# Optimization experiments

Measured on AMD Instinct MI355X. Metric: run time of the kernel, lower is better.

The kernel has to match this reference:

```python
import jax, jax.numpy as jnp
import numpy as np

B, S, E, H = 4, 512, 1024, 16
DH = E // H
SCALE = 1.0 / float(np.sqrt(DH))


def setup_inputs() -> dict:
    key = jax.random.key(0)
    ks = jax.random.split(key, 6)
    x_val = jax.random.normal(ks[0], (B, S, E), dtype=jnp.float32)
    eps = 0.1 * jax.random.uniform(ks[1], (B, S, E), dtype=jnp.float32)
    x_lb = x_val - eps
    x_ub = x_val + eps
    s = 1.0 / float(np.sqrt(E))
    in_proj_w = jax.random.uniform(ks[2], (E, 3 * E), jnp.float32, -s, s)
    in_proj_b = jax.random.uniform(ks[3], (3 * E,), jnp.float32, -s, s)
    out_proj_w = jax.random.uniform(ks[4], (E, E), jnp.float32, -s, s)
    out_proj_b = jax.random.uniform(ks[5], (E,), jnp.float32, -s, s)
    return dict(x_val=x_val, x_lb=x_lb, x_ub=x_ub,
                in_proj_w=in_proj_w, in_proj_b=in_proj_b,
                out_proj_w=out_proj_w, out_proj_b=out_proj_b)


def _pos(x):
    return jnp.maximum(x, 0.0)


def _neg(x):
    return jnp.minimum(x, 0.0)


def ibp_linear(v, l, u, W, b):
    # interval input x point weight: lb' = lb@W+ + ub@W-,  ub' = ub@W+ + lb@W-
    Wp, Wn = _pos(W), _neg(W)
    return v @ W + b, l @ Wp + u @ Wn + b, u @ Wp + l @ Wn + b


def ibp_matmul(av, al, au, bv, bl, bu):
    # interval x interval matmul with the 4-way clamp decomposition (as in ibp.matmul)
    val = av @ bv
    lb = (_pos(al) @ _pos(bl) + _pos(au) @ _neg(bl)
          + _neg(al) @ _pos(bu) + _neg(au) @ _neg(bu))
    ub = (_pos(au) @ _pos(bu) + _pos(al) @ _neg(bu)
          + _neg(au) @ _pos(bl) + _neg(al) @ _neg(bl))
    return val, lb, ub


def ibp_softmax(v, l, u):
    # p_i lower bound: exp(lb_i) / (exp(lb_i) + sum_{j!=i} exp(ub_j)); symmetric for upper
    pv = jax.nn.softmax(v, axis=-1)
    m = jnp.max(u, axis=-1, keepdims=True)
    e_l = jnp.exp(l - m)
    e_u = jnp.exp(u - m)
    S_l = jnp.sum(e_l, axis=-1, keepdims=True)
    S_u = jnp.sum(e_u, axis=-1, keepdims=True)
    pl = e_l / (S_u - e_u + e_l)
    pu = e_u / (S_l - e_l + e_u)
    return pv, jnp.clip(pl, 0.0, 1.0), jnp.clip(pu, 0.0, 1.0)


def _heads(x):  # [B,S,E] -> [B,H,S,DH]
    return x.reshape(B, S, H, DH).transpose(0, 2, 1, 3)


def _merge(x):  # [B,H,S,DH] -> [B,S,E]
    return x.transpose(0, 2, 1, 3).reshape(B, S, E)


def reference(x_val, x_lb, x_ub, in_proj_w, in_proj_b, out_proj_w, out_proj_b):
    qkv_v, qkv_l, qkv_u = ibp_linear(x_val, x_lb, x_ub, in_proj_w, in_proj_b)

    def split(t):
        q, k, v = jnp.split(t, 3, axis=-1)
        return _heads(q), _heads(k), _heads(v)

    (qv, kv, vv) = split(qkv_v)
    (ql, kl, vl) = split(qkv_l)
    (qu, ku, vu) = split(qkv_u)
    # positive scalar scale preserves bound ordering
    qv, ql, qu = qv * SCALE, ql * SCALE, qu * SCALE
    kT = lambda x: x.transpose(0, 1, 3, 2)
    sv, sl, su = ibp_matmul(qv, ql, qu, kT(kv), kT(kl), kT(ku))  # [B,H,S,S]
    pv, pl, pu = ibp_softmax(sv, sl, su)
    ov, ol, ou = ibp_matmul(pv, pl, pu, vv, vl, vu)  # [B,H,S,DH]
    ov, ol, ou = _merge(ov), _merge(ol), _merge(ou)
    yv, yl, yu = ibp_linear(ov, ol, ou, out_proj_w, out_proj_b)
    return jnp.stack([yv, yl, yu])  # [3,B,S,E]
```

## Files before the change

### kernel.cpp

```cpp
#include <hip/hip_runtime.h>
#include <math.h>

#define SEQ    512
#define EMB    1024
#define NHEAD  16
#define DHEAD  64
#define NBAT   4
#define QSCALE 0.125f
#define KS     72
#define VS     40

typedef __attribute__((ext_vector_type(8))) short bf16x8;
typedef __attribute__((ext_vector_type(4))) float f32x4;

#define MFMA16(a, b, c) __builtin_amdgcn_mfma_f32_16x16x32_bf16(a, b, c, 0, 0, 0)

__device__ __forceinline__ unsigned short f2b(float x) {
  union { float f; unsigned int u; } a; a.f = x;
  unsigned int u = a.u;
  unsigned int r = (u + 0x7fffu + ((u >> 16) & 1u)) >> 16;
  return (unsigned short)r;
}
__device__ __forceinline__ unsigned short f2b_fast(float x) {
  union { float f; unsigned int u; } a; a.f = x;
  return (unsigned short)((a.u + 0x8000u) >> 16);
}
__device__ __forceinline__ float b2f(unsigned short x) {
  union { unsigned int u; float f; } a; a.u = ((unsigned int)x) << 16; return a.f;
}

__device__ __forceinline__ void async16(const unsigned short* g, unsigned short* lds) {
  __builtin_amdgcn_global_load_lds(
      (const __attribute__((address_space(1))) unsigned int*)g,
      (__attribute__((address_space(3))) unsigned int*)lds, 16, 0, 0);
}

__device__ __forceinline__ void clamp_pn8(bf16x8 x, bf16x8* p, bf16x8* n) {
  const unsigned int* xu = (const unsigned int*)&x;
  unsigned int* pp = (unsigned int*)p;
  unsigned int* nn = (unsigned int*)n;
#pragma unroll
  for (int e = 0; e < 4; e++) {
    const unsigned int s = xu[e] & 0x80008000u;
    const unsigned int mask = s | (s - (s >> 15));
    nn[e] = xu[e] & mask;
    pp[e] = xu[e] & ~mask;
  }
}

__device__ __forceinline__ float wave16_sum(float x) {
#pragma unroll
  for (int m = 1; m <= 8; m <<= 1) x += __shfl_xor(x, m);
  return x;
}

__global__ __launch_bounds__(256)
void convert_stack(const float* __restrict__ v, const float* __restrict__ l,
                   const float* __restrict__ u,
                   unsigned short* __restrict__ outV,
                   unsigned short* __restrict__ outC,
                   unsigned short* __restrict__ outR, int total4)
{
  int i = blockIdx.x * 256 + threadIdx.x;
  if (i >= total4) return;
  float4 v4 = ((const float4*)v)[i];
  float4 l4 = ((const float4*)l)[i];
  float4 u4 = ((const float4*)u)[i];
  float lv[4] = {l4.x, l4.y, l4.z, l4.w};
  float uv[4] = {u4.x, u4.y, u4.z, u4.w};
  float vv[4] = {v4.x, v4.y, v4.z, v4.w};
  ushort4 ov, oc, orr;
  unsigned short* pv = (unsigned short*)&ov;
  unsigned short* pc = (unsigned short*)&oc;
  unsigned short* pr = (unsigned short*)&orr;
#pragma unroll
  for (int e = 0; e < 4; e++) {
    pv[e] = f2b(vv[e]);
    pc[e] = f2b(0.5f * (lv[e] + uv[e]));
    pr[e] = f2b(0.5f * (uv[e] - lv[e]));
  }
  ((ushort4*)outV)[i] = ov;
  ((ushort4*)outC)[i] = oc;
  ((ushort4*)outR)[i] = orr;
}

__global__ __launch_bounds__(256)
void wt_convert(const float* __restrict__ W,
                unsigned short* __restrict__ Wt,
                unsigned short* __restrict__ Wa, int K, int N)
{
  __shared__ float tile[32][33];
  const int n0 = blockIdx.x * 32, k0 = blockIdx.y * 32;
  const int tx = threadIdx.x, ty = threadIdx.y;
#pragma unroll
  for (int r = 0; r < 32; r += 8)
    tile[ty + r][tx] = W[(size_t)(k0 + ty + r) * N + n0 + tx];
  __syncthreads();
#pragma unroll
  for (int r = 0; r < 32; r += 8) {
    const float w = tile[tx][ty + r];
    const size_t o = (size_t)(n0 + ty + r) * K + k0 + tx;
    Wt[o] = f2b(w);
    Wa[o] = f2b(fabsf(w));
  }
}

template<int BN>
__global__ __launch_bounds__(256, 2)
void gemm_ibp3(const unsigned short* __restrict__ Av,
               const unsigned short* __restrict__ Ac,
               const unsigned short* __restrict__ Ar,
               const unsigned short* __restrict__ Bt,
               const unsigned short* __restrict__ Ba,
               int K, const float* __restrict__ bias,
               float* __restrict__ oV, float* __restrict__ oL, float* __restrict__ oU,
               unsigned short* __restrict__ hV, unsigned short* __restrict__ hL,
               unsigned short* __restrict__ hU,
               unsigned short* __restrict__ vtV, unsigned short* __restrict__ vtL,
               unsigned short* __restrict__ vtU, int N)
{
  constexpr int NF = BN / 32;
  __shared__ __attribute__((aligned(16))) unsigned short Avs[2][64 * 32];
  __shared__ __attribute__((aligned(16))) unsigned short Acs[2][64 * 32];
  __shared__ __attribute__((aligned(16))) unsigned short Ars[2][64 * 32];
  __shared__ __attribute__((aligned(16))) unsigned short Bts[2][BN * 32];
  __shared__ __attribute__((aligned(16))) unsigned short Bas[2][BN * 32];

  const int t = threadIdx.x, lane = t & 63, w = t >> 6;
  const int m0 = blockIdx.y * 64, n0 = blockIdx.x * BN;
  const int wm = w & 1, wn = w >> 1;
  const int quad = lane >> 4, r16 = lane & 15;
  const int srow = lane >> 2, sseg = lane & 3;

  f32x4 av[2][NF], ac[2][NF], ar[2][NF];
#pragma unroll
  for (int i = 0; i < 2; i++)
#pragma unroll
    for (int j = 0; j < NF; j++) {
      av[i][j] = (f32x4){0.f, 0.f, 0.f, 0.f};
      ac[i][j] = (f32x4){0.f, 0.f, 0.f, 0.f};
      ar[i][j] = (f32x4){0.f, 0.f, 0.f, 0.f};
    }

  const int iters = K >> 5;
  auto stage = [&](int it, int buf) {
    const int k0 = it * 32;
    const size_t ga = (size_t)(m0 + 16 * w + srow) * K + k0 + sseg * 8;
    async16(Av + ga, &Avs[buf][16 * w * 32]);
    async16(Ac + ga, &Acs[buf][16 * w * 32]);
    async16(Ar + ga, &Ars[buf][16 * w * 32]);
#pragma unroll
    for (int r = 0; r < BN / 64; r++) {
      const int brow = (BN / 4) * w + 16 * r;
      const size_t gb = (size_t)(n0 + brow + srow) * K + k0 + sseg * 8;
      async16(Bt + gb, &Bts[buf][brow * 32]);
      async16(Ba + gb, &Bas[buf][brow * 32]);
    }
  };

  stage(0, 0);
  for (int it = 0; it < iters; ++it) {
    const int cur = it & 1;
    __syncthreads();
    if (it + 1 < iters) stage(it + 1, cur ^ 1);
    bf16x8 fv[2], fc[2], fr[2], gt[NF], gb[NF];
#pragma unroll
    for (int i = 0; i < 2; i++) {
      const int off = (wm * 32 + i * 16 + r16) * 32 + quad * 8;
      fv[i] = *(const bf16x8*)(&Avs[cur][off]);
      fc[i] = *(const bf16x8*)(&Acs[cur][off]);
      fr[i] = *(const bf16x8*)(&Ars[cur][off]);
    }
#pragma unroll
    for (int j = 0; j < NF; j++) {
      const int off = (wn * (BN / 2) + j * 16 + r16) * 32 + quad * 8;
      gt[j] = *(const bf16x8*)(&Bts[cur][off]);
      gb[j] = *(const bf16x8*)(&Bas[cur][off]);
    }
#pragma unroll
    for (int i = 0; i < 2; i++)
#pragma unroll
      for (int j = 0; j < NF; j++) {
        av[i][j] = MFMA16(fv[i], gt[j], av[i][j]);
        ac[i][j] = MFMA16(fc[i], gt[j], ac[i][j]);
        ar[i][j] = MFMA16(fr[i], gb[j], ar[i][j]);
      }
  }

#pragma unroll
  for (int i = 0; i < 2; i++) {
    const int mbase = m0 + wm * 32 + i * 16 + quad * 4;
#pragma unroll
    for (int j = 0; j < NF; j++) {
      const int n = n0 + wn * (BN / 2) + j * 16 + r16;
      const float bv = bias[n];
      float vv[4], lv[4], uv[4];
#pragma unroll
      for (int rI = 0; rI < 4; rI++) {
        const float c = ac[i][j][rI], r = ar[i][j][rI];
        vv[rI] = av[i][j][rI] + bv;
        lv[rI] = c - r + bv;
        uv[rI] = c + r + bv;
      }
      if (hV) {
#pragma unroll
        for (int rI = 0; rI < 4; rI++) {
          hV[(size_t)(mbase + rI) * N + n] = f2b(vv[rI]);
          hL[(size_t)(mbase + rI) * N + n] = f2b(lv[rI]);
          hU[(size_t)(mbase + rI) * N + n] = f2b(uv[rI]);
        }
      } else {
#pragma unroll
        for (int rI = 0; rI < 4; rI++) {
          oV[(size_t)(mbase + rI) * N + n] = vv[rI];
          oL[(size_t)(mbase + rI) * N + n] = lv[rI];
          oU[(size_t)(mbase + rI) * N + n] = uv[rI];
        }
      }
      if (vtV && n >= 2048) {
        const int hh = (n - 2048) >> 6, dd = (n - 2048) & 63;
        const int bb = mbase >> 9, ss = mbase & 511;
        ushort4 v4, l4, u4;
        unsigned short* vp = (unsigned short*)&v4;
        unsigned short* lp = (unsigned short*)&l4;
        unsigned short* up = (unsigned short*)&u4;
#pragma unroll
        for (int rI = 0; rI < 4; rI++) {
          vp[rI] = f2b(vv[rI]); lp[rI] = f2b(lv[rI]); up[rI] = f2b(uv[rI]);
        }
        const size_t vo = (size_t)((bb * 16 + hh) * 64 + dd) * 512 + ss;
        *(ushort4*)(vtV + vo) = v4;
        *(ushort4*)(vtL + vo) = l4;
        *(ushort4*)(vtU + vo) = u4;
      }
    }
  }
}

__device__ __forceinline__ void qk_tile(const unsigned short* K0,
                                        const unsigned short* K1,
                                        const unsigned short* K2,
                                        int cl, int quad,
                                        const bf16x8 qvf[2], const bf16x8 qlpf[2],
                                        const bf16x8 qlnf[2], const bf16x8 qupf[2],
                                        const bf16x8 qunf[2],
                                        f32x4* avp, f32x4* alp, f32x4* aup)
{
  f32x4 v = {0.f, 0.f, 0.f, 0.f}, l = v, u = v;
#pragma unroll
  for (int kh = 0; kh < 2; kh++) {
    const int off = cl * KS + kh * 32 + quad * 8;
    bf16x8 kv = *(const bf16x8*)(K0 + off);
    bf16x8 kl = *(const bf16x8*)(K1 + off);
    bf16x8 ku = *(const bf16x8*)(K2 + off);
    bf16x8 klp, kln, kup, kun;
    clamp_pn8(kl, &klp, &kln);
    clamp_pn8(ku, &kup, &kun);
    v = MFMA16(qvf[kh], kv, v);
    l = MFMA16(qlpf[kh], klp, l);
    l = MFMA16(qupf[kh], kln, l);
    l = MFMA16(qlnf[kh], kup, l);
    l = MFMA16(qunf[kh], kun, l);
    u = MFMA16(qupf[kh], kup, u);
    u = MFMA16(qlpf[kh], kun, u);
    u = MFMA16(qunf[kh], klp, u);
    u = MFMA16(qlnf[kh], kln, u);
  }
  *avp = v; *alp = l; *aup = u;
}

__global__ __launch_bounds__(256, 4)
void ibp_attn_mfma(const unsigned short* __restrict__ qkv_v,
                   const unsigned short* __restrict__ qkv_l,
                   const unsigned short* __restrict__ qkv_u,
                   const unsigned short* __restrict__ vt_v,
                   const unsigned short* __restrict__ vt_l,
                   const unsigned short* __restrict__ vt_u,
                   unsigned short* __restrict__ Ov,
                   unsigned short* __restrict__ Oc,
                   unsigned short* __restrict__ Or)
{
  __shared__ __attribute__((aligned(16))) unsigned short pool[6912 + 7680 + 3840];
  __shared__ float st[2][32][3];
  unsigned short* Ks = pool;
  unsigned short* Vs = pool + 6912;
  unsigned short* Ps = pool + 6912 + 7680;

  const int qblk = blockIdx.x, h = blockIdx.y, b = blockIdx.z;
  const int t = threadIdx.x, lane = t & 63, w = t >> 6;
  const int wm = w >> 1, wc = w & 1;
  const int quad = lane >> 4, r16 = lane & 15;
  const int mq = b * SEQ + qblk * 32;
  const int bh = b * NHEAD + h;

  bf16x8 qvf[2], qlpf[2], qlnf[2], qupf[2], qunf[2];
  {
    const size_t qrow = (size_t)(mq + wm * 16 + r16) * 3072 + h * 64;
#pragma unroll
    for (int kh = 0; kh < 2; kh++) {
      bf16x8 v8 = *(const bf16x8*)(qkv_v + qrow + kh * 32 + quad * 8);
      bf16x8 l8 = *(const bf16x8*)(qkv_l + qrow + kh * 32 + quad * 8);
      bf16x8 u8 = *(const bf16x8*)(qkv_u + qrow + kh * 32 + quad * 8);
      const unsigned short* vs = (const unsigned short*)&v8;
      const unsigned short* ls = (const unsigned short*)&l8;
      const unsigned short* us = (const unsigned short*)&u8;
      unsigned short* ov = (unsigned short*)&qvf[kh];
      unsigned short* lp = (unsigned short*)&qlpf[kh];
      unsigned short* ln = (unsigned short*)&qlnf[kh];
      unsigned short* up = (unsigned short*)&qupf[kh];
      unsigned short* un = (unsigned short*)&qunf[kh];
#pragma unroll
      for (int e = 0; e < 8; e++) {
        ov[e] = f2b(b2f(vs[e]) * QSCALE);
        const float lf = b2f(ls[e]) * QSCALE;
        const float uf = b2f(us[e]) * QSCALE;
        lp[e] = f2b(fmaxf(lf, 0.f)); ln[e] = f2b(fminf(lf, 0.f));
        up[e] = f2b(fmaxf(uf, 0.f)); un[e] = f2b(fminf(uf, 0.f));
      }
    }
  }

  const int cl = wc * 16 + r16;
  const int krow = t >> 3, kseg = t & 7;
  const int vrow = t >> 2, vseg = t & 3;
  const unsigned short* kplane[3] = {qkv_v, qkv_l, qkv_u};
  const unsigned short* vplane[3] = {vt_v, vt_l, vt_u};

  float Svp[4] = {0.f, 0.f, 0.f, 0.f};
  float Slp[4] = {0.f, 0.f, 0.f, 0.f};
  float Sup[4] = {0.f, 0.f, 0.f, 0.f};

#pragma unroll
  for (int pI = 0; pI < 3; pI++)
    *(uint4*)(Ks + pI * 2304 + krow * KS + kseg * 8) =
        *(const uint4*)(kplane[pI] + (size_t)(b * SEQ + krow) * 3072 + 1024 + h * 64 + kseg * 8);
  __syncthreads();

  for (int ct = 0; ct < 16; ct++) {
    const unsigned short* cur = (ct & 1) ? Vs : Ks;
    if (ct < 15) {
      unsigned short* nxt = (ct & 1) ? Ks : Vs;
      const int c0n = (ct + 1) * 32;
#pragma unroll
      for (int pI = 0; pI < 3; pI++)
        *(uint4*)(nxt + pI * 2304 + krow * KS + kseg * 8) =
            *(const uint4*)(kplane[pI] + (size_t)(b * SEQ + c0n + krow) * 3072 + 1024 + h * 64 + kseg * 8);
    }
    f32x4 av, al, au;
    qk_tile(cur, cur + 2304, cur + 4608, cl, quad,
            qvf, qlpf, qlnf, qupf, qunf, &av, &al, &au);
#pragma unroll
    for (int r = 0; r < 4; r++) {
      Svp[r] += __expf(av[r]);
      Slp[r] += __expf(al[r]);
      Sup[r] += __expf(au[r]);
    }
    __syncthreads();
  }

#pragma unroll
  for (int r = 0; r < 4; r++) {
    Svp[r] = wave16_sum(Svp[r]);
    Slp[r] = wave16_sum(Slp[r]);
    Sup[r] = wave16_sum(Sup[r]);
  }
  if (r16 == 0) {
#pragma unroll
    for (int r = 0; r < 4; r++) {
      st[wc][wm * 16 + quad * 4 + r][0] = Svp[r];
      st[wc][wm * 16 + quad * 4 + r][1] = Slp[r];
      st[wc][wm * 16 + quad * 4 + r][2] = Sup[r];
    }
  }
  __syncthreads();
  float rSv4[4], Sl4[4], Su4[4];
#pragma unroll
  for (int r = 0; r < 4; r++) {
    const int row = wm * 16 + quad * 4 + r;
    rSv4[r] = 1.f / (st[0][row][0] + st[1][row][0]);
    Sl4[r]  = st[0][row][1] + st[1][row][1];
    Su4[r]  = st[0][row][2] + st[1][row][2];
  }

  f32x4 oa[3][2];
#pragma unroll
  for (int bo = 0; bo < 3; bo++)
#pragma unroll
    for (int ds = 0; ds < 2; ds++) oa[bo][ds] = (f32x4){0.f, 0.f, 0.f, 0.f};

  for (int ct = 0; ct < 16; ct++) {
    const int c0 = ct * 32;
    __syncthreads();
#pragma unroll
    for (int pI = 0; pI < 3; pI++) {
      *(uint4*)(Ks + pI * 2304 + krow * KS + kseg * 8) =
          *(const uint4*)(kplane[pI] + (size_t)(b * SEQ + c0 + krow) * 3072 + 1024 + h * 64 + kseg * 8);
      *(uint4*)(Vs + pI * 2560 + vrow * VS + vseg * 8) =
          *(const uint4*)(vplane[pI] + (size_t)(bh * 64 + vrow) * 512 + c0 + vseg * 8);
    }
    __syncthreads();

    f32x4 av, al, au;
    qk_tile(Ks, Ks + 2304, Ks + 4608, cl, quad,
            qvf, qlpf, qlnf, qupf, qunf, &av, &al, &au);
#pragma unroll
    for (int r = 0; r < 4; r++) {
      const float ev = __expf(av[r]);
      const float el = __expf(al[r]);
      const float eu = __expf(au[r]);
      float pl = el * __builtin_amdgcn_rcpf(Su4[r] - eu + el);
      float pu = eu * __builtin_amdgcn_rcpf(Sl4[r] - el + eu);
      pl = fminf(fmaxf(pl, 0.f), 1.f);
      pu = fminf(fmaxf(pu, 0.f), 1.f);
      const float pev = __shfl_xor(ev, 1);
      const float ppl = __shfl_xor(pl, 1);
      const float ppu = __shfl_xor(pu, 1);
      if (!(r16 & 1)) {
        const unsigned int wv = (unsigned int)f2b_fast(ev) | ((unsigned int)f2b_fast(pev) << 16);
        const unsigned int wl = (unsigned int)f2b_fast(pl) | ((unsigned int)f2b_fast(ppl) << 16);
        const unsigned int wu = (unsigned int)f2b_fast(pu) | ((unsigned int)f2b_fast(ppu) << 16);
        const int prow = (wm * 16 + quad * 4 + r) * VS + cl;
        *(unsigned int*)(Ps + prow)        = wv;
        *(unsigned int*)(Ps + 1280 + prow) = wl;
        *(unsigned int*)(Ps + 2560 + prow) = wu;
      }
    }
    __syncthreads();

#pragma unroll
    for (int ds = 0; ds < 2; ds++) {
      const int dsub = wc * 2 + ds;
      const int voff = (dsub * 16 + r16) * VS + quad * 8;
      bf16x8 vv = *(const bf16x8*)(Vs + voff);
      bf16x8 vl = *(const bf16x8*)(Vs + 2560 + voff);
      bf16x8 vu = *(const bf16x8*)(Vs + 5120 + voff);
      bf16x8 vlp, vln, vup, vun;
      clamp_pn8(vl, &vlp, &vln);
      clamp_pn8(vu, &vup, &vun);
      const int arow = (wm * 16 + r16) * VS + quad * 8;
      bf16x8 pav = *(const bf16x8*)(Ps + arow);
      bf16x8 pal = *(const bf16x8*)(Ps + 1280 + arow);
      bf16x8 pau = *(const bf16x8*)(Ps + 2560 + arow);
      oa[0][ds] = MFMA16(pav, vv, oa[0][ds]);
      oa[1][ds] = MFMA16(pal, vlp, oa[1][ds]);
      oa[1][ds] = MFMA16(pau, vln, oa[1][ds]);
      oa[2][ds] = MFMA16(pau, vup, oa[2][ds]);
      oa[2][ds] = MFMA16(pal, vun, oa[2][ds]);
    }
  }

#pragma unroll
  for (int ds = 0; ds < 2; ds++) {
    const int dsub = wc * 2 + ds;
#pragma unroll
    for (int r = 0; r < 4; r++) {
      const size_t row = (size_t)(mq + wm * 16 + quad * 4 + r);
      const int col = h * 64 + dsub * 16 + r16;
      const float ovv = oa[0][ds][r] * rSv4[r];
      const float olv = oa[1][ds][r];
      const float ouv = oa[2][ds][r];
      Ov[row * 1024 + col] = f2b(ovv);
      Oc[row * 1024 + col] = f2b(0.5f * (olv + ouv));
      Or[row * 1024 + col] = f2b(0.5f * (ouv - olv));
    }
  }
}

extern "C" void kernel_launch(void* const* d_in, const int* in_sizes, int n_in,
                              void* d_out, int out_size, void* d_ws, size_t ws_size,
                              hipStream_t stream)
{
  const float* x_val = (const float*)d_in[0];
  const float* x_lb  = (const float*)d_in[1];
  const float* x_ub  = (const float*)d_in[2];
  const float* Wi    = (const float*)d_in[3];
  const float* bi    = (const float*)d_in[4];
  const float* Wo    = (const float*)d_in[5];
  const float* bo    = (const float*)d_in[6];
  float* out = (float*)d_out;

  char* p = (char*)d_ws;
  unsigned short* Xv  = (unsigned short*)p; p += (size_t)2048 * 1024 * 2;
  unsigned short* Xc  = (unsigned short*)p; p += (size_t)2048 * 1024 * 2;
  unsigned short* Xr  = (unsigned short*)p; p += (size_t)2048 * 1024 * 2;
  unsigned short* Wit = (unsigned short*)p; p += (size_t)3072 * 1024 * 2;
  unsigned short* Wia = (unsigned short*)p; p += (size_t)3072 * 1024 * 2;
  unsigned short* Wot = (unsigned short*)p; p += (size_t)1024 * 1024 * 2;
  unsigned short* Woa = (unsigned short*)p; p += (size_t)1024 * 1024 * 2;
  unsigned short* qv  = (unsigned short*)p; p += (size_t)2048 * 3072 * 2;
  unsigned short* ql  = (unsigned short*)p; p += (size_t)2048 * 3072 * 2;
  unsigned short* qu  = (unsigned short*)p; p += (size_t)2048 * 3072 * 2;
  unsigned short* Vtv = (unsigned short*)p; p += (size_t)64 * 64 * 512 * 2;
  unsigned short* Vtl = (unsigned short*)p; p += (size_t)64 * 64 * 512 * 2;
  unsigned short* Vtu = (unsigned short*)p; p += (size_t)64 * 64 * 512 * 2;

  convert_stack<<<2048, 256, 0, stream>>>(x_val, x_lb, x_ub, Xv, Xc, Xr, 524288);
  wt_convert<<<dim3(96, 32), dim3(32, 8), 0, stream>>>(Wi, Wit, Wia, 1024, 3072);
  wt_convert<<<dim3(32, 32), dim3(32, 8), 0, stream>>>(Wo, Wot, Woa, 1024, 1024);

  gemm_ibp3<128><<<dim3(3072 / 128, 32), 256, 0, stream>>>(
      Xv, Xc, Xr, Wit, Wia, 1024, bi,
      nullptr, nullptr, nullptr, qv, ql, qu, Vtv, Vtl, Vtu, 3072);

  ibp_attn_mfma<<<dim3(SEQ / 32, NHEAD, NBAT), 256, 0, stream>>>(
      qv, ql, qu, Vtv, Vtl, Vtu, Xv, Xc, Xr);

  gemm_ibp3<64><<<dim3(1024 / 64, 32), 256, 0, stream>>>(
      Xv, Xc, Xr, Wot, Woa, 1024, bo,
      out, out + (size_t)2048 * 1024, out + (size_t)4096 * 1024,
      nullptr, nullptr, nullptr, nullptr, nullptr, nullptr, 1024);
}
```

Before: 314.5 us.

## Split attention into QK/exp kernel and PV kernel via materialized bf16 exps

The fused attention kernel, which seemingly computed the QK^T tile twice (once for row sums, once for probabilities), is replaced by two kernels. The first computes QK, exponentiates, stores bf16 exp values and row sums to workspace. The second reads them back, forms the softmax bounds and does the PV MFMA with double-buffered V tiles. This removes the recomputation of QK at the cost of writing and reading roughly 100MB of intermediates and an extra launch, and it falls back to the old kernel if the workspace is too small.

```diff
diff --git a/kernel.cpp b/kernel.cpp
--- a/kernel.cpp
+++ b/kernel.cpp
@@ -270,6 +270,295 @@
 }
 
 __global__ __launch_bounds__(256, 4)
+void ibp_attn_qk(const unsigned short* __restrict__ qkv_v,
+                 const unsigned short* __restrict__ qkv_l,
+                 const unsigned short* __restrict__ qkv_u,
+                 uint2* __restrict__ eVb, uint2* __restrict__ eLb,
+                 uint2* __restrict__ eUb, float4* __restrict__ sums)
+{
+  __shared__ __attribute__((aligned(16))) unsigned short Kd[2][3 * 2304];
+  __shared__ float st[2][32][3];
+
+  const int qblk = blockIdx.x, h = blockIdx.y, b = blockIdx.z;
+  const int t = threadIdx.x, lane = t & 63, w = t >> 6;
+  const int wm = w >> 1, wc = w & 1;
+  const int quad = lane >> 4, r16 = lane & 15;
+  const int mq = b * SEQ + qblk * 32;
+  const int bh = b * NHEAD + h;
+
+  bf16x8 qvf[2], qlpf[2], qlnf[2], qupf[2], qunf[2];
+  {
+    const size_t qrow = (size_t)(mq + wm * 16 + r16) * 3072 + h * 64;
+#pragma unroll
+    for (int kh = 0; kh < 2; kh++) {
+      bf16x8 v8 = *(const bf16x8*)(qkv_v + qrow + kh * 32 + quad * 8);
+      bf16x8 l8 = *(const bf16x8*)(qkv_l + qrow + kh * 32 + quad * 8);
+      bf16x8 u8 = *(const bf16x8*)(qkv_u + qrow + kh * 32 + quad * 8);
+      const unsigned short* vs = (const unsigned short*)&v8;
+      const unsigned short* ls = (const unsigned short*)&l8;
+      const unsigned short* us = (const unsigned short*)&u8;
+      unsigned short* ov = (unsigned short*)&qvf[kh];
+      unsigned short* lp = (unsigned short*)&qlpf[kh];
+      unsigned short* ln = (unsigned short*)&qlnf[kh];
+      unsigned short* up = (unsigned short*)&qupf[kh];
+      unsigned short* un = (unsigned short*)&qunf[kh];
+#pragma unroll
+      for (int e = 0; e < 8; e++) {
+        ov[e] = f2b(b2f(vs[e]) * QSCALE);
+        const float lf = b2f(ls[e]) * QSCALE;
+        const float uf = b2f(us[e]) * QSCALE;
+        lp[e] = f2b(fmaxf(lf, 0.f)); ln[e] = f2b(fminf(lf, 0.f));
+        up[e] = f2b(fmaxf(uf, 0.f)); un[e] = f2b(fminf(uf, 0.f));
+      }
+    }
+  }
+
+  const int cl = wc * 16 + r16;
+  const int krow = t >> 3, kseg = t & 7;
+
+  float Svp[4] = {0.f, 0.f, 0.f, 0.f};
+  float Slp[4] = {0.f, 0.f, 0.f, 0.f};
+  float Sup[4] = {0.f, 0.f, 0.f, 0.f};
+
+  uint4 kN0, kN1, kN2;
+  {
+    const size_t gk = (size_t)(b * SEQ + krow) * 3072 + 1024 + h * 64 + kseg * 8;
+    kN0 = *(const uint4*)(qkv_v + gk);
+    kN1 = *(const uint4*)(qkv_l + gk);
+    kN2 = *(const uint4*)(qkv_u + gk);
+    unsigned short* d = &Kd[0][krow * KS + kseg * 8];
+    *(uint4*)d = kN0;
+    *(uint4*)(d + 2304) = kN1;
+    *(uint4*)(d + 4608) = kN2;
+  }
+  __syncthreads();
+
+  const size_t ebase = (size_t)((bh * 16 + qblk) * 16) * 256 + t;
+
+  for (int ct = 0; ct < 16; ct++) {
+    const int cur = ct & 1;
+    if (ct < 15) {
+      const size_t gk = (size_t)(b * SEQ + (ct + 1) * 32 + krow) * 3072 + 1024
+                        + h * 64 + kseg * 8;
+      kN0 = *(const uint4*)(qkv_v + gk);
+      kN1 = *(const uint4*)(qkv_l + gk);
+      kN2 = *(const uint4*)(qkv_u + gk);
+    }
+    f32x4 av, al, au;
+    qk_tile(&Kd[cur][0], &Kd[cur][2304], &Kd[cur][4608], cl, quad,
+            qvf, qlpf, qlnf, qupf, qunf, &av, &al, &au);
+    float ev[4], el[4], eu[4];
+#pragma unroll
+    for (int r = 0; r < 4; r++) {
+      ev[r] = __expf(av[r]); Svp[r] += ev[r];
+      el[r] = __expf(al[r]); Slp[r] += el[r];
+      eu[r] = __expf(au[r]); Sup[r] += eu[r];
+    }
+    const size_t eo = ebase + (size_t)ct * 256;
+    uint2 d;
+    d.x = (unsigned int)f2b(ev[0]) | ((unsigned int)f2b(ev[1]) << 16);
+    d.y = (unsigned int)f2b(ev[2]) | ((unsigned int)f2b(ev[3]) << 16);
+    eVb[eo] = d;
+    d.x = (unsigned int)f2b(el[0]) | ((unsigned int)f2b(el[1]) << 16);
+    d.y = (unsigned int)f2b(el[2]) | ((unsigned int)f2b(el[3]) << 16);
+    eLb[eo] = d;
+    d.x = (unsigned int)f2b(eu[0]) | ((unsigned int)f2b(eu[1]) << 16);
+    d.y = (unsigned int)f2b(eu[2]) | ((unsigned int)f2b(eu[3]) << 16);
+    eUb[eo] = d;
+    if (ct < 15) {
+      unsigned short* dd = &Kd[cur ^ 1][krow * KS + kseg * 8];
+      *(uint4*)dd = kN0;
+      *(uint4*)(dd + 2304) = kN1;
+      *(uint4*)(dd + 4608) = kN2;
+      __syncthreads();
+    }
+  }
+
+#pragma unroll
+  for (int r = 0; r < 4; r++) {
+    Svp[r] = wave16_sum(Svp[r]);
+    Slp[r] = wave16_sum(Slp[r]);
+    Sup[r] = wave16_sum(Sup[r]);
+  }
+  if (r16 == 0) {
+#pragma unroll
+    for (int r = 0; r < 4; r++) {
+      st[wc][wm * 16 + quad * 4 + r][0] = Svp[r];
+      st[wc][wm * 16 + quad * 4 + r][1] = Slp[r];
+      st[wc][wm * 16 + quad * 4 + r][2] = Sup[r];
+    }
+  }
+  __syncthreads();
+  if (t < 32) {
+    float4 s;
+    s.x = st[0][t][0] + st[1][t][0];
+    s.y = st[0][t][1] + st[1][t][1];
+    s.z = st[0][t][2] + st[1][t][2];
+    s.w = 0.f;
+    sums[(size_t)bh * 512 + qblk * 32 + t] = s;
+  }
+}
+
+__global__ __launch_bounds__(256, 4)
+void ibp_attn_pv(const uint2* __restrict__ eVb, const uint2* __restrict__ eLb,
+                 const uint2* __restrict__ eUb, const float4* __restrict__ sums,
+                 const unsigned short* __restrict__ vt_v,
+                 const unsigned short* __restrict__ vt_l,
+                 const unsigned short* __restrict__ vt_u,
+                 unsigned short* __restrict__ Ov,
+                 unsigned short* __restrict__ Oc,
+                 unsigned short* __restrict__ Or)
+{
+  __shared__ __attribute__((aligned(16))) unsigned short Vd[2][3 * 2560];
+  __shared__ __attribute__((aligned(16))) unsigned short Ps[3 * 1280];
+
+  const int qblk = blockIdx.x, h = blockIdx.y, b = blockIdx.z;
+  const int t = threadIdx.x, lane = t & 63, w = t >> 6;
+  const int wm = w >> 1, wc = w & 1;
+  const int quad = lane >> 4, r16 = lane & 15;
+  const int mq = b * SEQ + qblk * 32;
+  const int bh = b * NHEAD + h;
+  const int cl = wc * 16 + r16;
+  const int vrow = t >> 2, vseg = t & 3;
+
+  float rSv4[4], Sl4[4], Su4[4];
+#pragma unroll
+  for (int r = 0; r < 4; r++) {
+    const float4 s = sums[(size_t)bh * 512 + qblk * 32 + wm * 16 + quad * 4 + r];
+    rSv4[r] = 1.f / s.x;
+    Sl4[r] = s.y;
+    Su4[r] = s.z;
+  }
+
+  const size_t ebase = (size_t)((bh * 16 + qblk) * 16) * 256 + t;
+  const size_t gvbase = (size_t)(bh * 64 + vrow) * 512 + vseg * 8;
+
+  uint4 vN0 = *(const uint4*)(vt_v + gvbase);
+  uint4 vN1 = *(const uint4*)(vt_l + gvbase);
+  uint4 vN2 = *(const uint4*)(vt_u + gvbase);
+  uint2 eC0 = eVb[ebase], eC1 = eLb[ebase], eC2 = eUb[ebase];
+  {
+    unsigned short* d = &Vd[0][vrow * VS + vseg * 8];
+    *(uint4*)d = vN0;
+    *(uint4*)(d + 2560) = vN1;
+    *(uint4*)(d + 5120) = vN2;
+  }
+  __syncthreads();
+
+  f32x4 oa[3][2];
+#pragma unroll
+  for (int bo = 0; bo < 3; bo++)
+#pragma unroll
+    for (int ds = 0; ds < 2; ds++) oa[bo][ds] = (f32x4){0.f, 0.f, 0.f, 0.f};
+
+  for (int ct = 0; ct < 16; ct++) {
+    const int cur = ct & 1;
+    uint2 eN0, eN1, eN2;
+    if (ct < 15) {
+      const size_t gv = gvbase + (ct + 1) * 32;
+      vN0 = *(const uint4*)(vt_v + gv);
+      vN1 = *(const uint4*)(vt_l + gv);
+      vN2 = *(const uint4*)(vt_u + gv);
+      const size_t eo = ebase + (size_t)(ct + 1) * 256;
+      eN0 = eVb[eo]; eN1 = eLb[eo]; eN2 = eUb[eo];
+    }
+
+    const unsigned int nvx = __shfl_xor(eC0.x, 1);
+    const unsigned int nvy = __shfl_xor(eC0.y, 1);
+    const float el0 = b2f((unsigned short)(eC1.x & 0xFFFFu));
+    const float el1 = b2f((unsigned short)(eC1.x >> 16));
+    const float el2 = b2f((unsigned short)(eC1.y & 0xFFFFu));
+    const float el3 = b2f((unsigned short)(eC1.y >> 16));
+    const float eu0 = b2f((unsigned short)(eC2.x & 0xFFFFu));
+    const float eu1 = b2f((unsigned short)(eC2.x >> 16));
+    const float eu2 = b2f((unsigned short)(eC2.y & 0xFFFFu));
+    const float eu3 = b2f((unsigned short)(eC2.y >> 16));
+    float pl[4], pu[4];
+    pl[0] = el0 * __builtin_amdgcn_rcpf(Su4[0] - eu0 + el0);
+    pu[0] = eu0 * __builtin_amdgcn_rcpf(Sl4[0] - el0 + eu0);
+    pl[1] = el1 * __builtin_amdgcn_rcpf(Su4[1] - eu1 + el1);
+    pu[1] = eu1 * __builtin_amdgcn_rcpf(Sl4[1] - el1 + eu1);
+    pl[2] = el2 * __builtin_amdgcn_rcpf(Su4[2] - eu2 + el2);
+    pu[2] = eu2 * __builtin_amdgcn_rcpf(Sl4[2] - el2 + eu2);
+    pl[3] = el3 * __builtin_amdgcn_rcpf(Su4[3] - eu3 + el3);
+    pu[3] = eu3 * __builtin_amdgcn_rcpf(Sl4[3] - el3 + eu3);
+#pragma unroll
+    for (int r = 0; r < 4; r++) {
+      pl[r] = fminf(fmaxf(pl[r], 0.f), 1.f);
+      pu[r] = fminf(fmaxf(pu[r], 0.f), 1.f);
+    }
+    const unsigned int dl0 = (unsigned int)f2b_fast(pl[0]) | ((unsigned int)f2b_fast(pl[1]) << 16);
+    const unsigned int dl1 = (unsigned int)f2b_fast(pl[2]) | ((unsigned int)f2b_fast(pl[3]) << 16);
+    const unsigned int du0 = (unsigned int)f2b_fast(pu[0]) | ((unsigned int)f2b_fast(pu[1]) << 16);
+    const unsigned int du1 = (unsigned int)f2b_fast(pu[2]) | ((unsigned int)f2b_fast(pu[3]) << 16);
+    const unsigned int nl0 = __shfl_xor(dl0, 1), nl1 = __shfl_xor(dl1, 1);
+    const unsigned int nu0 = __shfl_xor(du0, 1), nu1 = __shfl_xor(du1, 1);
+    if (!(r16 & 1)) {
+      const int rb = (wm * 16 + quad * 4) * VS + cl;
+      *(unsigned int*)(Ps + rb)               = (eC0.x & 0xFFFFu) | (nvx << 16);
+      *(unsigned int*)(Ps + rb + VS)          = (eC0.x >> 16) | (nvx & 0xFFFF0000u);
+      *(unsigned int*)(Ps + rb + 2 * VS)      = (eC0.y & 0xFFFFu) | (nvy << 16);
+      *(unsigned int*)(Ps + rb + 3 * VS)      = (eC0.y >> 16) | (nvy & 0xFFFF0000u);
+      *(unsigned int*)(Ps + 1280 + rb)          = (dl0 & 0xFFFFu) | (nl0 << 16);
+      *(unsigned int*)(Ps + 1280 + rb + VS)     = (dl0 >> 16) | (nl0 & 0xFFFF0000u);
+      *(unsigned int*)(Ps + 1280 + rb + 2 * VS) = (dl1 & 0xFFFFu) | (nl1 << 16);
+      *(unsigned int*)(Ps + 1280 + rb + 3 * VS) = (dl1 >> 16) | (nl1 & 0xFFFF0000u);
+      *(unsigned int*)(Ps + 2560 + rb)          = (du0 & 0xFFFFu) | (nu0 << 16);
+      *(unsigned int*)(Ps + 2560 + rb + VS)     = (du0 >> 16) | (nu0 & 0xFFFF0000u);
+      *(unsigned int*)(Ps + 2560 + rb + 2 * VS) = (du1 & 0xFFFFu) | (nu1 << 16);
+      *(unsigned int*)(Ps + 2560 + rb + 3 * VS) = (du1 >> 16) | (nu1 & 0xFFFF0000u);
+    }
+    __syncthreads();
+
+#pragma unroll
+    for (int ds = 0; ds < 2; ds++) {
+      const int dsub = wc * 2 + ds;
+      const int voff = (dsub * 16 + r16) * VS + quad * 8;
+      bf16x8 vv = *(const bf16x8*)(&Vd[cur][voff]);
+      bf16x8 vl = *(const bf16x8*)(&Vd[cur][2560 + voff]);
+      bf16x8 vu = *(const bf16x8*)(&Vd[cur][5120 + voff]);
+      bf16x8 vlp, vln, vup, vun;
+      clamp_pn8(vl, &vlp, &vln);
+      clamp_pn8(vu, &vup, &vun);
+      const int arow = (wm * 16 + r16) * VS + quad * 8;
+      bf16x8 pav = *(const bf16x8*)(Ps + arow);
+      bf16x8 pal = *(const bf16x8*)(Ps + 1280 + arow);
+      bf16x8 pau = *(const bf16x8*)(Ps + 2560 + arow);
+      oa[0][ds] = MFMA16(pav, vv, oa[0][ds]);
+      oa[1][ds] = MFMA16(pal, vlp, oa[1][ds]);
+      oa[1][ds] = MFMA16(pau, vln, oa[1][ds]);
+      oa[2][ds] = MFMA16(pau, vup, oa[2][ds]);
+      oa[2][ds] = MFMA16(pal, vun, oa[2][ds]);
+    }
+
+    if (ct < 15) {
+      unsigned short* d = &Vd[cur ^ 1][vrow * VS + vseg * 8];
+      *(uint4*)d = vN0;
+      *(uint4*)(d + 2560) = vN1;
+      *(uint4*)(d + 5120) = vN2;
+      eC0 = eN0; eC1 = eN1; eC2 = eN2;
+    }
+    __syncthreads();
+  }
+
+#pragma unroll
+  for (int ds = 0; ds < 2; ds++) {
+    const int dsub = wc * 2 + ds;
+#pragma unroll
+    for (int r = 0; r < 4; r++) {
+      const size_t row = (size_t)(mq + wm * 16 + quad * 4 + r);
+      const int col = h * 64 + dsub * 16 + r16;
+      const float ovv = oa[0][ds][r] * rSv4[r];
+      const float olv = oa[1][ds][r];
+      const float ouv = oa[2][ds][r];
+      Ov[row * 1024 + col] = f2b(ovv);
+      Oc[row * 1024 + col] = f2b(0.5f * (olv + ouv));
+      Or[row * 1024 + col] = f2b(0.5f * (ouv - olv));
+    }
+  }
+}
+
+__global__ __launch_bounds__(256, 4)
 void ibp_attn_mfma(const unsigned short* __restrict__ qkv_v,
                    const unsigned short* __restrict__ qkv_l,
                    const unsigned short* __restrict__ qkv_u,
@@ -284,7 +573,7 @@
   __shared__ float st[2][32][3];
   unsigned short* Ks = pool;
   unsigned short* Vs = pool + 6912;
-  unsigned short* Ps = pool + 6912 + 7680;
+  unsigned short* Psl = pool + 6912 + 7680;
 
   const int qblk = blockIdx.x, h = blockIdx.y, b = blockIdx.z;
   const int t = threadIdx.x, lane = t & 63, w = t >> 6;
@@ -420,9 +709,9 @@
         const unsigned int wl = (unsigned int)f2b_fast(pl) | ((unsigned int)f2b_fast(ppl) << 16);
         const unsigned int wu = (unsigned int)f2b_fast(pu) | ((unsigned int)f2b_fast(ppu) << 16);
         const int prow = (wm * 16 + quad * 4 + r) * VS + cl;
-        *(unsigned int*)(Ps + prow)        = wv;
-        *(unsigned int*)(Ps + 1280 + prow) = wl;
-        *(unsigned int*)(Ps + 2560 + prow) = wu;
+        *(unsigned int*)(Psl + prow)        = wv;
+        *(unsigned int*)(Psl + 1280 + prow) = wl;
+        *(unsigned int*)(Psl + 2560 + prow) = wu;
       }
     }
     __syncthreads();
@@ -438,9 +727,9 @@
       clamp_pn8(vl, &vlp, &vln);
       clamp_pn8(vu, &vup, &vun);
       const int arow = (wm * 16 + r16) * VS + quad * 8;
-      bf16x8 pav = *(const bf16x8*)(Ps + arow);
-      bf16x8 pal = *(const bf16x8*)(Ps + 1280 + arow);
-      bf16x8 pau = *(const bf16x8*)(Ps + 2560 + arow);
+      bf16x8 pav = *(const bf16x8*)(Psl + arow);
+      bf16x8 pal = *(const bf16x8*)(Psl + 1280 + arow);
+      bf16x8 pau = *(const bf16x8*)(Psl + 2560 + arow);
       oa[0][ds] = MFMA16(pav, vv, oa[0][ds]);
       oa[1][ds] = MFMA16(pal, vlp, oa[1][ds]);
       oa[1][ds] = MFMA16(pau, vln, oa[1][ds]);
@@ -493,6 +782,11 @@
   unsigned short* Vtv = (unsigned short*)p; p += (size_t)64 * 64 * 512 * 2;
   unsigned short* Vtl = (unsigned short*)p; p += (size_t)64 * 64 * 512 * 2;
   unsigned short* Vtu = (unsigned short*)p; p += (size_t)64 * 64 * 512 * 2;
+  uint2* eVb = (uint2*)p;  p += (size_t)1024 * 16 * 256 * 8;
+  uint2* eLb = (uint2*)p;  p += (size_t)1024 * 16 * 256 * 8;
+  uint2* eUb = (uint2*)p;  p += (size_t)1024 * 16 * 256 * 8;
+  float4* sums = (float4*)p; p += (size_t)64 * 512 * 16;
+  const size_t need = (size_t)(p - (char*)d_ws);
 
   convert_stack<<<2048, 256, 0, stream>>>(x_val, x_lb, x_ub, Xv, Xc, Xr, 524288);
   wt_convert<<<dim3(96, 32), dim3(32, 8), 0, stream>>>(Wi, Wit, Wia, 1024, 3072);
@@ -502,8 +796,15 @@
       Xv, Xc, Xr, Wit, Wia, 1024, bi,
       nullptr, nullptr, nullptr, qv, ql, qu, Vtv, Vtl, Vtu, 3072);
 
-  ibp_attn_mfma<<<dim3(SEQ / 32, NHEAD, NBAT), 256, 0, stream>>>(
-      qv, ql, qu, Vtv, Vtl, Vtu, Xv, Xc, Xr);
+  if (ws_size >= need) {
+    ibp_attn_qk<<<dim3(SEQ / 32, NHEAD, NBAT), 256, 0, stream>>>(
+        qv, ql, qu, eVb, eLb, eUb, sums);
+    ibp_attn_pv<<<dim3(SEQ / 32, NHEAD, NBAT), 256, 0, stream>>>(
+        eVb, eLb, eUb, sums, Vtv, Vtl, Vtu, Xv, Xc, Xr);
+  } else {
+    ibp_attn_mfma<<<dim3(SEQ / 32, NHEAD, NBAT), 256, 0, stream>>>(
+        qv, ql, qu, Vtv, Vtl, Vtu, Xv, Xc, Xr);
+  }
 
   gemm_ibp3<64><<<dim3(1024 / 64, 32), 256, 0, stream>>>(
       Xv, Xc, Xr, Wot, Woa, 1024, bo,
```

Result: faster. 288.4 us (-8.3%).
